# Kernel optimization log

Measured on AMD Instinct MI355X. Metric: run time of the kernel, lower is better.

Reference implementation:

```python
import jax, jax.numpy as jnp
import numpy as np

D_MODEL, HEADS, GROUPS, DIM_HEAD = 256, 8, 8, 64
INNER = HEADS * DIM_HEAD              # 512
OFF_DIMS = INNER // GROUPS            # 64 channels fed to the offset network per group
DF, OFF_SCALE, KS, PAD = 4, 4.0, 6, 1  # downsample_factor, offset_scale, kernel, (6-4)//2
CPB_DIM = D_MODEL // 4                # 64
NUM_LAYERS = 6
SCALE = DIM_HEAD ** -0.5
B, H, W = 1, 40, 40


def grouped_conv1x1(x, w, g):
    # x: (b, cin, h, w); w: (cout, cin//g) torch grouped 1x1 conv weight (squeezed)
    b, cin, h, wd = x.shape
    cout = w.shape[0]
    xg = x.reshape(b, g, cin // g, h, wd)
    wg = w.reshape(g, cout // g, cin // g)
    return jnp.einsum('goi,bgihw->bgohw', wg, xg).reshape(b, cout, h, wd)


def create_grid(h, w, dtype):
    # torch meshgrid(arange(w), arange(h), indexing='xy') stacked at dim 0
    ys, xs = jnp.meshgrid(jnp.arange(h, dtype=dtype), jnp.arange(w, dtype=dtype), indexing='ij')
    return jnp.stack((xs, ys))  # (2, h, w): channel0 = x, channel1 = y


def normalize_grid(grid):
    # faithful to source: channel0 scaled by (h-1), channel1 by (w-1); out dim last
    h, w = grid.shape[-2:]
    g0 = 2.0 * grid[..., 0, :, :] / max(h - 1, 1) - 1.0
    g1 = 2.0 * grid[..., 1, :, :] / max(w - 1, 1) - 1.0
    return jnp.stack((g0, g1), axis=-1)


def grid_sample_bilinear(img, grid):
    # torch F.grid_sample, mode='bilinear', padding_mode='zeros', align_corners=False
    Bn, C, Hh, Ww = img.shape
    gx = ((grid[..., 0] + 1.0) * Ww - 1.0) * 0.5
    gy = ((grid[..., 1] + 1.0) * Hh - 1.0) * 0.5
    x0 = jnp.floor(gx)
    y0 = jnp.floor(gy)
    wx1 = gx - x0
    wy1 = gy - y0
    flat = img.reshape(Bn, C, Hh * Ww)

    def gather(xi, yi):
        valid = (xi >= 0) & (xi <= Ww - 1) & (yi >= 0) & (yi <= Hh - 1)
        xc = jnp.clip(xi, 0, Ww - 1).astype(jnp.int32)
        yc = jnp.clip(yi, 0, Hh - 1).astype(jnp.int32)
        idx = (yc * Ww + xc).reshape(Bn, 1, -1)
        vals = jnp.take_along_axis(flat, idx, axis=2).reshape(Bn, C, *xi.shape[1:])
        return vals * valid[:, None].astype(img.dtype)

    return (gather(x0, y0) * ((1 - wx1) * (1 - wy1))[:, None]
            + gather(x0 + 1, y0) * (wx1 * (1 - wy1))[:, None]
            + gather(x0, y0 + 1) * ((1 - wx1) * wy1)[:, None]
            + gather(x0 + 1, y0 + 1) * (wx1 * wy1)[:, None])


def deform_attn(x, wq, wk, wv, w_off1, b_off1, w_off2,
                cpb_w0, cpb_b0, cpb_w1, cpb_b1, cpb_w2, cpb_b2, w_out, b_out):
    b, c, Hh, Ww = x.shape
    bg = b * GROUPS
    q = grouped_conv1x1(x, wq, GROUPS)                      # (b, 512, H, W)
    qg = q.reshape(bg, OFF_DIMS, Hh, Ww)                    # group heads: (b g) d h w
    # offset network: depthwise 6x6 stride-4 conv -> GELU -> 1x1 -> tanh * scale
    off = jax.lax.conv_general_dilated(
        qg, w_off1, (DF, DF), ((PAD, PAD), (PAD, PAD)),
        dimension_numbers=('NCHW', 'OIHW', 'NCHW'), feature_group_count=OFF_DIMS)
    off = jax.nn.gelu(off + b_off1[None, :, None, None], approximate=False)
    off = jnp.tanh(jnp.einsum('oc,bchw->bohw', w_off2, off)) * OFF_SCALE  # (bg,2,h',w')
    hp, wp = off.shape[-2:]
    vgrid = create_grid(hp, wp, x.dtype)[None] + off
    vgrid_scaled = normalize_grid(vgrid)                    # (bg, h', w', 2)
    xg = x.reshape(bg, c // GROUPS, Hh, Ww)
    kv = grid_sample_bilinear(xg, vgrid_scaled).reshape(b, c, hp, wp)
    k = grouped_conv1x1(kv, wk, GROUPS)
    v = grouped_conv1x1(kv, wv, GROUPS)
    i, j = Hh * Ww, hp * wp
    qh = (q * SCALE).reshape(b, HEADS, DIM_HEAD, i).transpose(0, 1, 3, 2)  # bhid
    kh = k.reshape(b, HEADS, DIM_HEAD, j).transpose(0, 1, 3, 2)
    vh = v.reshape(b, HEADS, DIM_HEAD, j).transpose(0, 1, 3, 2)
    sim = jnp.einsum('bhid,bhjd->bhij', qh, kh)
    # continuous positional bias (CPB, depth-2 MLP on signed-log relative coords)
    grid_q = normalize_grid(create_grid(Hh, Ww, x.dtype)).reshape(i, 2)
    grid_kv = vgrid_scaled.reshape(bg, j, 2)
    pos = grid_q[None, :, None, :] - grid_kv[:, None, :, :]  # (bg, i, j, 2)
    bias = jnp.sign(pos) * jnp.log1p(jnp.abs(pos))
    bias = jax.nn.relu(bias @ cpb_w0.T + cpb_b0)
    bias = jax.nn.relu(bias @ cpb_w1.T + cpb_b1)
    bias = bias @ cpb_w2.T + cpb_b2                          # (bg, i, j, 1)
    sim = sim + bias.reshape(b, GROUPS, i, j)                # heads//offset_groups == 1
    attn = jax.nn.softmax(sim, axis=-1)                      # stable softmax (matches amax-subtract)
    out = jnp.einsum('bhij,bhjd->bhid', attn, vh)
    out = out.transpose(0, 1, 3, 2).reshape(b, INNER, Hh, Ww)
    return jnp.einsum('oc,bchw->bohw', w_out, out) + b_out[None, :, None, None]


def setup_inputs() -> dict:
    key = jax.random.key(0)
    ks = jax.random.split(key, 16)
    L = NUM_LAYERS

    def p(k, shape, scale=0.02):
        return jax.random.normal(k, shape, dtype=jnp.float32) * scale

    return {
        'bev_feat': jax.random.normal(ks[0], (B, D_MODEL, H, W), dtype=jnp.float32),
        'wq': p(ks[1], (L, INNER, D_MODEL // GROUPS)),
        'wk': p(ks[2], (L, INNER, D_MODEL // GROUPS)),
        'wv': p(ks[3], (L, INNER, D_MODEL // GROUPS)),
        'w_off1': p(ks[4], (L, OFF_DIMS, 1, KS, KS)),
        'b_off1': jnp.zeros((L, OFF_DIMS), jnp.float32),
        'w_off2': p(ks[5], (L, 2, OFF_DIMS)),
        'cpb_w0': p(ks[6], (L, CPB_DIM, 2), 0.5),
        'cpb_b0': jnp.zeros((L, CPB_DIM), jnp.float32),
        'cpb_w1': p(ks[7], (L, CPB_DIM, CPB_DIM), 0.1),
        'cpb_b1': jnp.zeros((L, CPB_DIM), jnp.float32),
        'cpb_w2': p(ks[8], (L, 1, CPB_DIM), 0.1),
        'cpb_b2': jnp.zeros((L, 1), jnp.float32),
        'w_out': p(ks[9], (L, D_MODEL, INNER)),
        'b_out': jnp.zeros((L, D_MODEL), jnp.float32),
    }


def reference(bev_feat, wq, wk, wv, w_off1, b_off1, w_off2,
              cpb_w0, cpb_b0, cpb_w1, cpb_b1, cpb_w2, cpb_b2, w_out, b_out):
    # The source encoder loop runs `output = layer(bev_feat)` on the ORIGINAL
    # input each iteration, so only the last layer's output survives. Faithful
    # math = apply layer NUM_LAYERS-1 once (dropout in eval mode -> identity).
    l = NUM_LAYERS - 1
    return deform_attn(bev_feat, wq[l], wk[l], wv[l], w_off1[l], b_off1[l], w_off2[l],
                       cpb_w0[l], cpb_b0[l], cpb_w1[l], cpb_b1[l], cpb_w2[l], cpb_b2[l],
                       w_out[l], b_out[l])
```

## Files before the change

kernel.cpp:

```cpp
#include <hip/hip_runtime.h>
#include <math.h>


#define NP 1600
#define NJ 100

typedef _Float16 f16x8 __attribute__((ext_vector_type(8)));
typedef _Float16 f16x4 __attribute__((ext_vector_type(4)));
typedef _Float16 f16x2 __attribute__((ext_vector_type(2)));
typedef float  f32x4  __attribute__((ext_vector_type(4)));
typedef float  f32x2  __attribute__((ext_vector_type(2)));

template<int CTRL>
__device__ __forceinline__ float dpp_add(float x) {
  int y = __builtin_amdgcn_update_dpp(0, __builtin_bit_cast(int, x),
                                      CTRL, 0xf, 0xf, true);
  return x + __builtin_bit_cast(float, y);
}

__global__ __launch_bounds__(256) void k_conv1x1(
    const float* __restrict__ x, const float* __restrict__ w,
    float* __restrict__ out, float* __restrict__ out_t) {
  int b = blockIdx.x;
  int g = b / 40;
  int r = b - g * 40;
  int oc = r / 5;
  int p0 = (r - oc * 5) * 320;
  int co0 = g * 64 + oc * 8;
  const float* xg = x + g * 32 * NP;
  const float* wr = w + co0 * 32;
  for (int p = p0 + threadIdx.x; p < p0 + 320; p += 256) {
    float acc[8];
#pragma unroll
    for (int o = 0; o < 8; ++o) acc[o] = 0.f;
#pragma unroll
    for (int ci = 0; ci < 32; ++ci) {
      float xv = xg[ci * NP + p];
#pragma unroll
      for (int o = 0; o < 8; ++o) acc[o] = fmaf(wr[o * 32 + ci], xv, acc[o]);
    }
#pragma unroll
    for (int o = 0; o < 8; ++o) out[(co0 + o) * NP + p] = acc[o];
    f32x4 t0, t1;
    t0[0] = acc[0]; t0[1] = acc[1]; t0[2] = acc[2]; t0[3] = acc[3];
    t1[0] = acc[4]; t1[1] = acc[5]; t1[2] = acc[6]; t1[3] = acc[7];
    *(f32x4*)(out_t + (size_t)p * 512 + co0) = t0;
    *(f32x4*)(out_t + (size_t)p * 512 + co0 + 4) = t1;
  }
}

__global__ __launch_bounds__(256, 4) void k_off_cpb(
    const float* __restrict__ qt, const float* __restrict__ wdw,
    const float* __restrict__ bdw, const float* __restrict__ wo2,
    const float* __restrict__ x, const float* __restrict__ wk,
    const float* __restrict__ wv,
    const float* __restrict__ w0, const float* __restrict__ b0,
    const float* __restrict__ w1, const float* __restrict__ b1v,
    const float* __restrict__ cw2, const float* __restrict__ b2,
    float* __restrict__ kout, float* __restrict__ vout_t,
    _Float16* __restrict__ bias16) {
  __shared__ float psum[4][72];
  __shared__ float su_l[40];
  __shared__ float sv_l[40];
  __shared__ _Float16 a16[40][72];
  __shared__ _Float16 c16[40][72];
  int b = blockIdx.x;
  int g = b & 7;
  int j = b >> 3;
  int gj = g * 100 + j;
  int t = threadIdx.x;
  int lane = t & 63;
  int wv_id = t >> 6;
  int oy = j / 10, ox = j - (j / 10) * 10;
  int row = lane & 15;
  int kgrp = lane >> 4;

  {
    float acc = 0.f;
    const float* qrow = qt + g * 64 + lane;
#pragma unroll
    for (int tu = 0; tu < 9; ++tu) {
      int tt = wv_id * 9 + tu;
      int ky = tt / 6, kx = tt - (tt / 6) * 6;
      int iy = oy * 4 - 1 + ky;
      int ix = ox * 4 - 1 + kx;
      if (iy >= 0 && iy < 40 && ix >= 0 && ix < 40)
        acc = fmaf(wdw[lane * 36 + tt], qrow[(size_t)(iy * 40 + ix) * 512], acc);
    }
    psum[wv_id][lane] = acc;
  }
  __syncthreads();

  if (wv_id == 0) {
    float accd = psum[0][lane] + psum[1][lane] + psum[2][lane] + psum[3][lane]
               + bdw[lane];
    float od = 0.5f * accd * (1.0f + erff(accd * 0.70710678118654752440f));
    float px = wo2[lane] * od, py = wo2[64 + lane] * od;
#pragma unroll
    for (int m = 1; m < 64; m <<= 1) {
      px += __shfl_xor(px, m);
      py += __shfl_xor(py, m);
    }
    float ax = tanhf(px) * 4.f;
    float ay = tanhf(py) * 4.f;
    float vx = (float)ox + ax;
    float vy = (float)oy + ay;
    float g0 = 2.f * vx / 9.f - 1.f;
    float g1 = 2.f * vy / 9.f - 1.f;
    if (lane < 40) {
      float qc = (float)lane * (2.f / 39.f) - 1.f;
      float u = qc - g0;
      float vv2 = qc - g1;
      su_l[lane] = copysignf(log1pf(fabsf(u)), u);
      sv_l[lane] = copysignf(log1pf(fabsf(vv2)), vv2);
    }
    float gx = ((g0 + 1.f) * 40.f - 1.f) * 0.5f;
    float gy = ((g1 + 1.f) * 40.f - 1.f) * 0.5f;
    float x0f = floorf(gx), y0f = floorf(gy);
    float wx = gx - x0f, wy = gy - y0f;
    bool mx0 = (x0f >= 0.f) && (x0f <= 39.f);
    bool mx1 = (x0f + 1.f >= 0.f) && (x0f + 1.f <= 39.f);
    bool my0 = (y0f >= 0.f) && (y0f <= 39.f);
    bool my1 = (y0f + 1.f >= 0.f) && (y0f + 1.f <= 39.f);
    int ix0 = (int)fminf(fmaxf(x0f, 0.f), 39.f);
    int ix1 = (int)fminf(fmaxf(x0f + 1.f, 0.f), 39.f);
    int iy0 = (int)fminf(fmaxf(y0f, 0.f), 39.f);
    int iy1 = (int)fminf(fmaxf(y0f + 1.f, 0.f), 39.f);
    float w00 = (1.f - wx) * (1.f - wy) * ((mx0 && my0) ? 1.f : 0.f);
    float w10 = wx * (1.f - wy) * ((mx1 && my0) ? 1.f : 0.f);
    float w01 = (1.f - wx) * wy * ((mx0 && my1) ? 1.f : 0.f);
    float w11 = wx * wy * ((mx1 && my1) ? 1.f : 0.f);
    int b00 = iy0 * 40 + ix0, b10 = iy0 * 40 + ix1;
    int b01 = iy1 * 40 + ix0, b11 = iy1 * 40 + ix1;
    float kvc = 0.f;
    if (lane < 32) {
      const float* xc = x + (g * 32 + lane) * NP;
      kvc = w00 * xc[b00] + w10 * xc[b10] + w01 * xc[b01] + w11 * xc[b11];
    }
    const float* wkr = wk + (g * 64 + lane) * 32;
    const float* wvr = wv + (g * 64 + lane) * 32;
    float wkreg[32], wvreg[32];
#pragma unroll
    for (int q4 = 0; q4 < 8; ++q4) {
      f32x4 a = *(const f32x4*)(wkr + q4 * 4);
      f32x4 bq = *(const f32x4*)(wvr + q4 * 4);
#pragma unroll
      for (int e = 0; e < 4; ++e) { wkreg[q4 * 4 + e] = a[e]; wvreg[q4 * 4 + e] = bq[e]; }
    }
    float kacc = 0.f, vacc = 0.f;
#pragma unroll
    for (int c = 0; c < 32; ++c) {
      float kvb = __shfl(kvc, c);
      kacc = fmaf(wkreg[c], kvb, kacc);
      vacc = fmaf(wvreg[c], kvb, vacc);
    }
    kout[(g * 64 + lane) * 100 + j] = kacc;
    vout_t[(size_t)gj * 64 + lane] = vacc;
  }
  __syncthreads();

  for (int idx = t; idx < 2560; idx += 256) {
    int xi = idx >> 6, kk = idx & 63;
    a16[xi][kk] = (_Float16)fmaf(w0[2 * kk], su_l[xi], b0[kk]);
    c16[xi][kk] = (_Float16)(w0[2 * kk + 1] * sv_l[xi]);
  }

  f16x8 B[4][2];
#pragma unroll
  for (int ct = 0; ct < 4; ++ct)
#pragma unroll
    for (int s = 0; s < 2; ++s)
#pragma unroll
      for (int e = 0; e < 8; ++e)
        B[ct][s][e] = (_Float16)w1[(ct * 16 + row) * 64 + s * 32 + kgrp * 8 + e];
  float b1c[4], w2c[4];
#pragma unroll
  for (int ct = 0; ct < 4; ++ct) {
    b1c[ct] = b1v[ct * 16 + row];
    w2c[ct] = cw2[ct * 16 + row];
  }
  float bb = b2[0];
  _Float16* outp = bias16 + (size_t)gj * 1600;
  __syncthreads();

  int it0 = wv_id * 25;
  int iy = wv_id * 10;
  int ix = row;
  f16x8 zero8 = {};
  for (int it = it0; it < it0 + 25; ++it) {
    f32x4 acc[4];
#pragma unroll
    for (int ct = 0; ct < 4; ++ct) {
      acc[ct][0] = 0.f; acc[ct][1] = 0.f; acc[ct][2] = 0.f; acc[ct][3] = 0.f;
    }
#pragma unroll
    for (int s = 0; s < 2; ++s) {
      f16x8 av = *(const f16x8*)&a16[ix][s * 32 + kgrp * 8];
      f16x8 cv = *(const f16x8*)&c16[iy][s * 32 + kgrp * 8];
      f16x8 A = __builtin_elementwise_max(av + cv, zero8);
#pragma unroll
      for (int ct = 0; ct < 4; ++ct)
        acc[ct] = __builtin_amdgcn_mfma_f32_16x16x32_f16(A, B[ct][s], acc[ct], 0, 0, 0);
    }
    float part[4];
#pragma unroll
    for (int ri = 0; ri < 4; ++ri) {
      float s2 = 0.f;
#pragma unroll
      for (int ct = 0; ct < 4; ++ct) {
        float val = acc[ct][ri] + b1c[ct];
        s2 = fmaf(w2c[ct], fmaxf(val, 0.f), s2);
      }
      part[ri] = s2;
    }
#pragma unroll
    for (int ri = 0; ri < 4; ++ri) {
      part[ri] = dpp_add<0xB1>(part[ri]);
      part[ri] = dpp_add<0x4E>(part[ri]);
      part[ri] = dpp_add<0x141>(part[ri]);
      part[ri] = dpp_add<0x140>(part[ri]);
    }
    if (row == 0) {
      f16x4 o;
      o[0] = (_Float16)(part[0] + bb); o[1] = (_Float16)(part[1] + bb);
      o[2] = (_Float16)(part[2] + bb); o[3] = (_Float16)(part[3] + bb);
      *(f16x4*)(outp + it * 16 + kgrp * 4) = o;
    }
    ix += 16;
    if (ix >= 40) { ix -= 40; ++iy; }
  }
}

__global__ __launch_bounds__(256) void k_attn(
    const float* __restrict__ q, const float* __restrict__ k,
    const float* __restrict__ v_t, const _Float16* __restrict__ bias16,
    float* __restrict__ inner) {
  __shared__ float v_lds[100][68];
  __shared__ float s_lds[16][100];
  int h = blockIdx.x / 100;
  int i0 = (blockIdx.x - h * 100) * 16;
  int t = threadIdx.x;
  for (int idx = t; idx < 6400; idx += 256) {
    int j = idx >> 6, d = idx & 63;
    v_lds[j][d] = v_t[(size_t)h * 6400 + idx];
  }
  __syncthreads();
  if (t < 200) {
    int ib = (t / 25) * 2, jb = (t % 25) * 4;
    const float* qp = q + h * 64 * NP + i0 + ib;
    const float* kp = k + h * 64 * 100 + jb;
    float a[2][4];
#pragma unroll
    for (int ii = 0; ii < 2; ++ii)
#pragma unroll
      for (int jj = 0; jj < 4; ++jj) a[ii][jj] = 0.f;
#pragma unroll 8
    for (int d = 0; d < 64; ++d) {
      f32x2 qv = *(const f32x2*)(qp + d * NP);
      f32x4 kv4 = *(const f32x4*)(kp + d * 100);
#pragma unroll
      for (int ii = 0; ii < 2; ++ii)
#pragma unroll
        for (int jj = 0; jj < 4; ++jj)
          a[ii][jj] = fmaf(qv[ii], kv4[jj], a[ii][jj]);
    }
    const _Float16* bcol = bias16 + (size_t)h * 100 * 1600;
#pragma unroll
    for (int jj = 0; jj < 4; ++jj) {
      f16x2 bv = *(const f16x2*)(bcol + (size_t)(jb + jj) * 1600 + i0 + ib);
#pragma unroll
      for (int ii = 0; ii < 2; ++ii)
        s_lds[ib + ii][jb + jj] = fmaf(a[ii][jj], 0.125f, (float)bv[ii]);
    }
  }
  __syncthreads();
  {
    int i = t >> 4, sub = t & 15;
    float m = -1e30f;
    for (int j = sub; j < 100; j += 16) m = fmaxf(m, s_lds[i][j]);
#pragma unroll
    for (int off = 1; off < 16; off <<= 1) m = fmaxf(m, __shfl_xor(m, off));
    float sum = 0.f;
    for (int j = sub; j < 100; j += 16) {
      float e = expf(s_lds[i][j] - m);
      s_lds[i][j] = e;
      sum += e;
    }
#pragma unroll
    for (int off = 1; off < 16; off <<= 1) sum += __shfl_xor(sum, off);
    float inv = 1.f / sum;
    for (int j = sub; j < 100; j += 16) s_lds[i][j] *= inv;
  }
  __syncthreads();
  {
    int i = t & 15, db = (t >> 4) * 4;
    float acc[4];
#pragma unroll
    for (int dd = 0; dd < 4; ++dd) acc[dd] = 0.f;
    for (int jc = 0; jc < 25; ++jc) {
      f32x4 sv = *(const f32x4*)&s_lds[i][jc * 4];
#pragma unroll
      for (int jj = 0; jj < 4; ++jj) {
        f32x4 vv = *(const f32x4*)&v_lds[jc * 4 + jj][db];
#pragma unroll
        for (int dd = 0; dd < 4; ++dd)
          acc[dd] = fmaf(sv[jj], vv[dd], acc[dd]);
      }
    }
#pragma unroll
    for (int dd = 0; dd < 4; ++dd)
      inner[(h * 64 + db + dd) * NP + i0 + i] = acc[dd];
  }
}

__global__ __launch_bounds__(256) void k_proj(
    const float* __restrict__ inner, const float* __restrict__ w,
    const float* __restrict__ bo, float* __restrict__ out) {
  int oc = blockIdx.x & 31;
  int pt = blockIdx.x >> 5;
  int t = threadIdx.x;
  int quad = __builtin_amdgcn_readfirstlane(t >> 6);
  int o0 = oc * 8 + quad * 2;
  int p = pt * 64 + (t & 63);
  const float* w0r = w + (size_t)o0 * 512;
  float a0 = 0.f, a1 = 0.f;
#pragma unroll 8
  for (int c = 0; c < 512; ++c) {
    float xv = inner[c * NP + p];
    a0 = fmaf(w0r[c], xv, a0);
    a1 = fmaf(w0r[512 + c], xv, a1);
  }
  out[(o0 + 0) * NP + p] = a0 + bo[o0 + 0];
  out[(o0 + 1) * NP + p] = a1 + bo[o0 + 1];
}

extern "C" void kernel_launch(void* const* d_in, const int* in_sizes, int n_in,
                              void* d_out, int out_size, void* d_ws, size_t ws_size,
                              hipStream_t stream) {
  int L = in_sizes[1] / (512 * 32);
  int l = L - 1;
  const float* x      = (const float*)d_in[0];
  const float* wq     = (const float*)d_in[1]  + (size_t)l * 512 * 32;
  const float* wk     = (const float*)d_in[2]  + (size_t)l * 512 * 32;
  const float* wv     = (const float*)d_in[3]  + (size_t)l * 512 * 32;
  const float* w_off1 = (const float*)d_in[4]  + (size_t)l * 64 * 36;
  const float* b_off1 = (const float*)d_in[5]  + (size_t)l * 64;
  const float* w_off2 = (const float*)d_in[6]  + (size_t)l * 2 * 64;
  const float* cpb_w0 = (const float*)d_in[7]  + (size_t)l * 64 * 2;
  const float* cpb_b0 = (const float*)d_in[8]  + (size_t)l * 64;
  const float* cpb_w1 = (const float*)d_in[9]  + (size_t)l * 64 * 64;
  const float* cpb_b1 = (const float*)d_in[10] + (size_t)l * 64;
  const float* cpb_w2 = (const float*)d_in[11] + (size_t)l * 64;
  const float* cpb_b2 = (const float*)d_in[12] + (size_t)l * 1;
  const float* w_out  = (const float*)d_in[13] + (size_t)l * 256 * 512;
  const float* b_out  = (const float*)d_in[14] + (size_t)l * 256;
  float* out = (float*)d_out;

  float* ws = (float*)d_ws;
  float*    q_ws    = ws;
  float*    qt_ws   = ws + 819200;
  float*    k_ws    = ws + 1638400;
  float*    vt_ws   = ws + 1689600;
  _Float16* bias16  = (_Float16*)(ws + 1740800);
  float*    inner   = ws + 2380800;

  k_conv1x1<<<320, 256, 0, stream>>>(x, wq, q_ws, qt_ws);
  k_off_cpb<<<800, 256, 0, stream>>>(qt_ws, w_off1, b_off1, w_off2, x, wk, wv,
                                     cpb_w0, cpb_b0, cpb_w1, cpb_b1, cpb_w2,
                                     cpb_b2, k_ws, vt_ws, bias16);
  k_attn<<<800, 256, 0, stream>>>(q_ws, k_ws, vt_ws, bias16, inner);
  k_proj<<<800, 256, 0, stream>>>(inner, w_out, b_out, out);
}
```

Baseline: 98.98 us.

## Fuse query 1x1 projection into offset and attention kernels, drop conv kernel

```diff
diff --git a/kernel.cpp b/kernel.cpp
--- a/kernel.cpp
+++ b/kernel.cpp
@@ -18,42 +18,11 @@
   return x + __builtin_bit_cast(float, y);
 }
 
-__global__ __launch_bounds__(256) void k_conv1x1(
-    const float* __restrict__ x, const float* __restrict__ w,
-    float* __restrict__ out, float* __restrict__ out_t) {
-  int b = blockIdx.x;
-  int g = b / 40;
-  int r = b - g * 40;
-  int oc = r / 5;
-  int p0 = (r - oc * 5) * 320;
-  int co0 = g * 64 + oc * 8;
-  const float* xg = x + g * 32 * NP;
-  const float* wr = w + co0 * 32;
-  for (int p = p0 + threadIdx.x; p < p0 + 320; p += 256) {
-    float acc[8];
-#pragma unroll
-    for (int o = 0; o < 8; ++o) acc[o] = 0.f;
-#pragma unroll
-    for (int ci = 0; ci < 32; ++ci) {
-      float xv = xg[ci * NP + p];
-#pragma unroll
-      for (int o = 0; o < 8; ++o) acc[o] = fmaf(wr[o * 32 + ci], xv, acc[o]);
-    }
-#pragma unroll
-    for (int o = 0; o < 8; ++o) out[(co0 + o) * NP + p] = acc[o];
-    f32x4 t0, t1;
-    t0[0] = acc[0]; t0[1] = acc[1]; t0[2] = acc[2]; t0[3] = acc[3];
-    t1[0] = acc[4]; t1[1] = acc[5]; t1[2] = acc[6]; t1[3] = acc[7];
-    *(f32x4*)(out_t + (size_t)p * 512 + co0) = t0;
-    *(f32x4*)(out_t + (size_t)p * 512 + co0 + 4) = t1;
-  }
-}
-
 __global__ __launch_bounds__(256, 4) void k_off_cpb(
-    const float* __restrict__ qt, const float* __restrict__ wdw,
+    const float* __restrict__ x, const float* __restrict__ wq,
+    const float* __restrict__ wdw,
     const float* __restrict__ bdw, const float* __restrict__ wo2,
-    const float* __restrict__ x, const float* __restrict__ wk,
-    const float* __restrict__ wv,
+    const float* __restrict__ wk, const float* __restrict__ wv,
     const float* __restrict__ w0, const float* __restrict__ b0,
     const float* __restrict__ w1, const float* __restrict__ b1v,
     const float* __restrict__ cw2, const float* __restrict__ b2,
@@ -76,16 +45,30 @@
   int kgrp = lane >> 4;
 
   {
+    float wqreg[32];
+    const float* wqr = wq + (size_t)(g * 64 + lane) * 32;
+#pragma unroll
+    for (int q4 = 0; q4 < 8; ++q4) {
+      f32x4 a = *(const f32x4*)(wqr + q4 * 4);
+#pragma unroll
+      for (int e = 0; e < 4; ++e) wqreg[q4 * 4 + e] = a[e];
+    }
+    const float* xg = x + g * 32 * NP;
     float acc = 0.f;
-    const float* qrow = qt + g * 64 + lane;
 #pragma unroll
     for (int tu = 0; tu < 9; ++tu) {
       int tt = wv_id * 9 + tu;
       int ky = tt / 6, kx = tt - (tt / 6) * 6;
       int iy = oy * 4 - 1 + ky;
       int ix = ox * 4 - 1 + kx;
-      if (iy >= 0 && iy < 40 && ix >= 0 && ix < 40)
-        acc = fmaf(wdw[lane * 36 + tt], qrow[(size_t)(iy * 40 + ix) * 512], acc);
+      if (iy >= 0 && iy < 40 && ix >= 0 && ix < 40) {
+        int pix = iy * 40 + ix;
+        float qv = 0.f;
+#pragma unroll
+        for (int ci = 0; ci < 32; ++ci)
+          qv = fmaf(wqreg[ci], xg[ci * NP + pix], qv);
+        acc = fmaf(wdw[lane * 36 + tt], qv, acc);
+      }
     }
     psum[wv_id][lane] = acc;
   }
@@ -232,11 +215,12 @@
 }
 
 __global__ __launch_bounds__(256) void k_attn(
-    const float* __restrict__ q, const float* __restrict__ k,
-    const float* __restrict__ v_t, const _Float16* __restrict__ bias16,
-    float* __restrict__ inner) {
+    const float* __restrict__ x, const float* __restrict__ wq,
+    const float* __restrict__ k, const float* __restrict__ v_t,
+    const _Float16* __restrict__ bias16, float* __restrict__ inner) {
   __shared__ float v_lds[100][68];
   __shared__ float s_lds[16][100];
+  __shared__ float q_lds[64][20];
   int h = blockIdx.x / 100;
   int i0 = (blockIdx.x - h * 100) * 16;
   int t = threadIdx.x;
@@ -244,10 +228,26 @@
     int j = idx >> 6, d = idx & 63;
     v_lds[j][d] = v_t[(size_t)h * 6400 + idx];
   }
+  {
+    int d = t & 63;
+    int i4 = t >> 6;
+    f32x4 wr[8];
+#pragma unroll
+    for (int qq = 0; qq < 8; ++qq)
+      wr[qq] = *(const f32x4*)(wq + (size_t)(h * 64 + d) * 32 + qq * 4);
+#pragma unroll
+    for (int ii = 0; ii < 4; ++ii) {
+      int i = i4 * 4 + ii;
+      float acc = 0.f;
+#pragma unroll
+      for (int ci = 0; ci < 32; ++ci)
+        acc = fmaf(wr[ci >> 2][ci & 3], x[(h * 32 + ci) * NP + i0 + i], acc);
+      q_lds[d][i] = acc;
+    }
+  }
   __syncthreads();
   if (t < 200) {
     int ib = (t / 25) * 2, jb = (t % 25) * 4;
-    const float* qp = q + h * 64 * NP + i0 + ib;
     const float* kp = k + h * 64 * 100 + jb;
     float a[2][4];
 #pragma unroll
@@ -256,7 +256,7 @@
       for (int jj = 0; jj < 4; ++jj) a[ii][jj] = 0.f;
 #pragma unroll 8
     for (int d = 0; d < 64; ++d) {
-      f32x2 qv = *(const f32x2*)(qp + d * NP);
+      f32x2 qv = *(const f32x2*)&q_lds[d][ib];
       f32x4 kv4 = *(const f32x4*)(kp + d * 100);
 #pragma unroll
       for (int ii = 0; ii < 2; ++ii)
@@ -357,17 +357,14 @@
   float* out = (float*)d_out;
 
   float* ws = (float*)d_ws;
-  float*    q_ws    = ws;
-  float*    qt_ws   = ws + 819200;
-  float*    k_ws    = ws + 1638400;
-  float*    vt_ws   = ws + 1689600;
-  _Float16* bias16  = (_Float16*)(ws + 1740800);
-  float*    inner   = ws + 2380800;
-
-  k_conv1x1<<<320, 256, 0, stream>>>(x, wq, q_ws, qt_ws);
-  k_off_cpb<<<800, 256, 0, stream>>>(qt_ws, w_off1, b_off1, w_off2, x, wk, wv,
+  float*    k_ws    = ws;
+  float*    vt_ws   = ws + 51200;
+  _Float16* bias16  = (_Float16*)(ws + 102400);
+  float*    inner   = ws + 742400;
+
+  k_off_cpb<<<800, 256, 0, stream>>>(x, wq, w_off1, b_off1, w_off2, wk, wv,
                                      cpb_w0, cpb_b0, cpb_w1, cpb_b1, cpb_w2,
                                      cpb_b2, k_ws, vt_ws, bias16);
-  k_attn<<<800, 256, 0, stream>>>(q_ws, k_ws, vt_ws, bias16, inner);
+  k_attn<<<800, 256, 0, stream>>>(x, wq, k_ws, vt_ws, bias16, inner);
   k_proj<<<800, 256, 0, stream>>>(inner, w_out, b_out, out);
 }
```

Result: no change. 99.56 us (+0.6%).
